# Kernel optimization log

Measured on AMD Instinct MI355X. Metric: run time of the kernel, lower is better.

Reference implementation:

```python
import jax, jax.numpy as jnp
import numpy as np

T, K, E, D, F = 2048, 6, 32, 2048, 1408   # tokens, top_k, routed experts, dim, moe_inter_dim
S = 2                                      # fused shared experts
C = T * K // E                             # exact per-expert capacity (balanced routing)


def _silu_and_mul(gu):
    # merged gate_up activation: silu(gate_half) * up_half
    g, u = jnp.split(gu, 2, axis=-1)
    return jax.nn.silu(g) * u


def setup_inputs() -> dict:
    key = jax.random.key(0)
    ks = jax.random.split(key, 7)
    x = jax.random.normal(ks[0], (T, D), dtype=jnp.float32)
    # balanced routing: every expert receives exactly C = T*K/E token-expert pairs
    indices = jax.random.permutation(ks[1], jnp.arange(T * K, dtype=jnp.int32) % E).reshape(T, K)
    weights = jax.random.uniform(ks[2], (T, K), dtype=jnp.float32)
    scale = 0.02
    w_gate_up = jax.random.normal(ks[3], (E, D, 2 * F), dtype=jnp.float32) * scale
    w_down = jax.random.normal(ks[4], (E, F, D), dtype=jnp.float32) * scale
    w_gate_up_shared = jax.random.normal(ks[5], (S, D, 2 * F), dtype=jnp.float32) * scale
    w_down_shared = jax.random.normal(ks[6], (S, F, D), dtype=jnp.float32) * scale
    return {"x": x, "weights": weights, "w_gate_up": w_gate_up, "w_down": w_down,
            "w_gate_up_shared": w_gate_up_shared, "w_down_shared": w_down_shared,
            "indices": indices}


def reference(x, weights, w_gate_up, w_down, w_gate_up_shared, w_down_shared, indices):
    # ---- dispatch: sort token-expert pairs by expert id (balanced -> exactly C per expert)
    flat_e = indices.reshape(-1)                       # [T*K]
    order = jnp.argsort(flat_e, stable=True)           # [T*K] pair ids grouped by expert
    tok = order // K                                   # source token of each sorted pair
    w_sorted = weights.reshape(-1)[order]              # routing weight of each sorted pair
    xg = x[tok].reshape(E, C, D)                       # gathered per-expert inputs
    # ---- routed experts: grouped gate_up GEMM -> silu_and_mul -> down GEMM
    act = _silu_and_mul(jnp.einsum('ecd,edf->ecf', xg, w_gate_up))   # [E, C, F]
    down = jnp.einsum('ecf,efd->ecd', act, w_down)                   # [E, C, D]
    # ---- combine: weighted scatter-add back to token order (y[idx] += out * weights[idx, top])
    y = jnp.zeros_like(x).at[tok].add(down.reshape(E * C, D) * w_sorted[:, None])
    # ---- fused shared experts: run on all tokens, added unweighted
    act_s = _silu_and_mul(jnp.einsum('td,sdf->stf', x, w_gate_up_shared))  # [S, T, F]
    y = y + jnp.einsum('stf,sfd->td', act_s, w_down_shared)
    return y
```

## Files before the change

kernel.cpp:

```cpp
#include <hip/hip_runtime.h>
#include <hip/hip_bf16.h>

#define TT 2048
#define KK 6
#define EE 32
#define DD 2048
#define FF 1408
#define SS 2
#define CC 384

typedef __bf16 bf16_t;
typedef __attribute__((ext_vector_type(8))) __bf16 bf16x8;
typedef __attribute__((ext_vector_type(4))) float f32x4;
typedef unsigned int u32;

#define AS1 __attribute__((address_space(1)))
#define AS3 __attribute__((address_space(3)))

__device__ __forceinline__ u32 f2bf(float f) {
    u32 u = __builtin_bit_cast(u32, f);
    return (u + 0x7fffu + ((u >> 16) & 1u)) >> 16;
}
__device__ __forceinline__ u32 pack2(float a, float b) {
    return f2bf(a) | (f2bf(b) << 16);
}
__device__ __forceinline__ float silu_mul(float g, float u) {
    return (g / (1.0f + __expf(-g))) * u;
}

__global__ void k_dispatch(const int* __restrict__ idx, int* __restrict__ counts,
                           int* __restrict__ tok, int* __restrict__ sop) {
    int p = blockIdx.x * 256 + threadIdx.x;
    if (p >= TT * KK) return;
    int e = idx[p];
    int pos = atomicAdd(&counts[e], 1);
    int slot = e * CC + pos;
    tok[slot] = p / KK;
    sop[p] = slot;
}

__global__ void k_gather(const float* __restrict__ x, const int* __restrict__ tok,
                         bf16_t* __restrict__ xall) {
    int row = blockIdx.x;
    int srow = (row < EE * CC) ? tok[row] : (row - EE * CC);
    const float* src = x + (size_t)srow * DD;
    bf16_t* dst = xall + (size_t)row * DD;
    int c0 = threadIdx.x * 8;
    float4 a = *(const float4*)(src + c0);
    float4 b = *(const float4*)(src + c0 + 4);
    uint4 o;
    o.x = pack2(a.x, a.y); o.y = pack2(a.z, a.w);
    o.z = pack2(b.x, b.y); o.w = pack2(b.z, b.w);
    *(uint4*)(dst + c0) = o;
}

#define BSTR 40

__device__ __forceinline__ void stage_a6(const bf16_t* __restrict__ A, int Kdim, int k0,
                                         bf16_t* dst, int arow, int ac, int wid) {
    #pragma unroll
    for (int i = 0; i < 6; ++i) {
        const int row = i * 64 + arow;
        const int cs = ac ^ ((row >> 1) & 3);
        const bf16_t* g = A + (size_t)row * Kdim + (k0 + cs * 8);
        AS3 u32* l = (AS3 u32*)(void*)(dst + (size_t)(i * 64 + wid * 16) * 32);
        __builtin_amdgcn_global_load_lds((const AS1 u32*)(const void*)g, l, 16, 0, 0);
    }
}

template<bool FUSED>
__global__ __launch_bounds__(256) void k_gemm_r(
    const bf16_t* __restrict__ Aall, const float* __restrict__ Br,
    bf16_t* __restrict__ Out, int Kdim, int Bstr, int Ostr, int NB)
{
    const int lin = blockIdx.x;
    const int xcd = lin & 7, jj = lin >> 3;
    const int e = xcd + 8 * (jj / NB);
    const int nblk = jj % NB;

    const bf16_t* A = Aall + (size_t)e * CC * Kdim;
    const float* Bbase = Br + (size_t)e * Kdim * Bstr;

    const int tid = threadIdx.x;
    const int lane = tid & 63, wid = tid >> 6;
    const int m_base = wid * 96;
    const int l15 = lane & 15, lq = lane >> 4;
    const int arow = tid >> 2, ac = tid & 3;
    const int kb = (tid >> 6) * 8;
    const int bn = tid & 63;

    const float* bsrc;
    bf16_t* Cout;
    if (FUSED) {
        const float* Bg = Bbase + nblk * 32;
        bsrc = (((tid >> 5) & 1) ? (Bg + FF) : Bg) + (tid & 31);
        Cout = Out + (size_t)e * CC * Ostr + nblk * 32;
    } else {
        bsrc = Bbase + nblk * 64 + bn;
        Cout = Out + (size_t)e * CC * Ostr + nblk * 64;
    }

    __shared__ __align__(16) bf16_t As[2][CC * 32];
    __shared__ __align__(16) bf16_t Bs[2][64 * BSTR];

    f32x4 acc[6][4] = {};
    const int ksteps = Kdim >> 5;

    auto loadB = [&](int k0, float* v) {
        const float* sp = bsrc + (size_t)(k0 + kb) * Bstr;
        #pragma unroll
        for (int t = 0; t < 8; ++t) v[t] = sp[(size_t)t * Bstr];
    };
    auto writeB = [&](int b, const float* v) {
        uint4 w;
        w.x = pack2(v[0], v[1]); w.y = pack2(v[2], v[3]);
        w.z = pack2(v[4], v[5]); w.w = pack2(v[6], v[7]);
        *(uint4*)(&Bs[b][0] + (size_t)bn * BSTR + kb) = w;
    };

    {
        stage_a6(A, Kdim, 0, &As[0][0], arow, ac, wid);
        float v[8]; loadB(0, v); writeB(0, v);
    }
    __syncthreads();

    int cur = 0;
    for (int kt = 0; kt < ksteps; ++kt) {
        const bool pf = (kt + 1 < ksteps);
        float vn[8];
        if (pf) {
            const int k1 = (kt + 1) << 5;
            stage_a6(A, Kdim, k1, &As[cur ^ 1][0], arow, ac, wid);
            loadB(k1, vn);
        }
        bf16x8 bfr[4];
        #pragma unroll
        for (int j = 0; j < 4; ++j)
            bfr[j] = *(const bf16x8*)(&Bs[cur][0] + (size_t)(j * 16 + l15) * BSTR + lq * 8);
        #pragma unroll
        for (int m = 0; m < 6; ++m) {
            const int row = m_base + m * 16 + l15;
            bf16x8 af = *(const bf16x8*)(&As[cur][0] + (size_t)row * 32 + (size_t)((lq ^ ((row >> 1) & 3)) * 8));
            #pragma unroll
            for (int j = 0; j < 4; ++j)
                acc[m][j] = __builtin_amdgcn_mfma_f32_16x16x32_bf16(af, bfr[j], acc[m][j], 0, 0, 0);
        }
        if (pf) writeB(cur ^ 1, vn);
        __syncthreads();
        cur ^= 1;
    }

    if (FUSED) {
        #pragma unroll
        for (int m = 0; m < 6; ++m)
            #pragma unroll
            for (int j = 0; j < 2; ++j) {
                const int n = j * 16 + l15;
                #pragma unroll
                for (int r = 0; r < 4; ++r) {
                    const int mm = m_base + m * 16 + lq * 4 + r;
                    Cout[(size_t)mm * Ostr + n] = (bf16_t)silu_mul(acc[m][j][r], acc[m][j + 2][r]);
                }
            }
    } else {
        #pragma unroll
        for (int m = 0; m < 6; ++m)
            #pragma unroll
            for (int j = 0; j < 4; ++j) {
                const int n = j * 16 + l15;
                #pragma unroll
                for (int r = 0; r < 4; ++r) {
                    const int mm = m_base + m * 16 + lq * 4 + r;
                    Cout[(size_t)mm * Ostr + n] = (bf16_t)acc[m][j][r];
                }
            }
    }
}

template<bool FUSED>
__global__ __launch_bounds__(256) void k_gemm_s(
    const bf16_t* __restrict__ Ash, const float* __restrict__ Bsh,
    bf16_t* __restrict__ Out, int Kdim, int Bstr, int Ostr, int ash_stride)
{
    const int s = blockIdx.z;
    const int n0 = blockIdx.x * (FUSED ? 64 : 128);
    const bf16_t* A = Ash + ((size_t)s * ash_stride + (size_t)blockIdx.y * 128) * Kdim;
    bf16_t* Cout = Out + ((size_t)s * TT + (size_t)blockIdx.y * 128) * Ostr + n0;
    const float* Bbase = Bsh + (size_t)s * Kdim * Bstr + n0;

    const int tid = threadIdx.x;
    const int lane = tid & 63, wid = tid >> 6;
    const int m_off = (wid >> 1) * 64, wn = wid & 1;
    const int l15 = lane & 15, lq = lane >> 4;
    const int arow = tid >> 2, ac = tid & 3;
    const int bn = tid & 127, kb = (tid >> 7) * 16;

    const float* bsrc;
    if (FUSED) bsrc = (((tid >> 6) & 1) ? (Bbase + FF) : Bbase) + (tid & 63);
    else       bsrc = Bbase + bn;

    __shared__ __align__(16) bf16_t As[2][128 * 32];
    __shared__ __align__(16) bf16_t Bs[2][128 * BSTR];

    f32x4 acc[4][4] = {};
    const int ksteps = Kdim >> 5;

    auto stageA = [&](int b, int k0) {
        const int cs = ac ^ ((arow >> 1) & 3);
        const bf16_t* g0 = A + (size_t)arow * Kdim + (k0 + cs * 8);
        const bf16_t* g1 = A + (size_t)(arow + 64) * Kdim + (k0 + cs * 8);
        AS3 u32* l0 = (AS3 u32*)(void*)(&As[b][0] + (size_t)(wid * 16) * 32);
        AS3 u32* l1 = (AS3 u32*)(void*)(&As[b][0] + (size_t)(64 + wid * 16) * 32);
        __builtin_amdgcn_global_load_lds((const AS1 u32*)(const void*)g0, l0, 16, 0, 0);
        __builtin_amdgcn_global_load_lds((const AS1 u32*)(const void*)g1, l1, 16, 0, 0);
    };
    auto loadB = [&](int k0, float* v) {
        const float* sp = bsrc + (size_t)(k0 + kb) * Bstr;
        #pragma unroll
        for (int t = 0; t < 16; ++t) v[t] = sp[(size_t)t * Bstr];
    };
    auto writeB = [&](int b, const float* v) {
        u32 p[8];
        #pragma unroll
        for (int t = 0; t < 8; ++t) p[t] = pack2(v[2 * t], v[2 * t + 1]);
        uint4 w0, w1;
        w0.x = p[0]; w0.y = p[1]; w0.z = p[2]; w0.w = p[3];
        w1.x = p[4]; w1.y = p[5]; w1.z = p[6]; w1.w = p[7];
        *(uint4*)(&Bs[b][0] + (size_t)bn * BSTR + kb) = w0;
        *(uint4*)(&Bs[b][0] + (size_t)bn * BSTR + kb + 8) = w1;
    };

    {
        stageA(0, 0);
        float v[16]; loadB(0, v); writeB(0, v);
    }
    __syncthreads();

    int cur = 0;
    for (int kt = 0; kt < ksteps; ++kt) {
        const bool pf = (kt + 1 < ksteps);
        float vn[16];
        if (pf) {
            const int k1 = (kt + 1) << 5;
            stageA(cur ^ 1, k1);
            loadB(k1, vn);
        }
        bf16x8 af[4], bfr[4];
        #pragma unroll
        for (int i = 0; i < 4; ++i) {
            const int row = m_off + i * 16 + l15;
            af[i] = *(const bf16x8*)(&As[cur][0] + (size_t)row * 32 + (size_t)((lq ^ ((row >> 1) & 3)) * 8));
        }
        #pragma unroll
        for (int j = 0; j < 4; ++j) {
            const int n_ds = FUSED ? (wn * 32 + (j & 1) * 16 + (j >> 1) * 64)
                                   : (wn * 64 + j * 16);
            bfr[j] = *(const bf16x8*)(&Bs[cur][0] + (size_t)(n_ds + l15) * BSTR + lq * 8);
        }
        #pragma unroll
        for (int i = 0; i < 4; ++i)
            #pragma unroll
            for (int j = 0; j < 4; ++j)
                acc[i][j] = __builtin_amdgcn_mfma_f32_16x16x32_bf16(af[i], bfr[j], acc[i][j], 0, 0, 0);
        if (pf) writeB(cur ^ 1, vn);
        __syncthreads();
        cur ^= 1;
    }

    if (FUSED) {
        #pragma unroll
        for (int i = 0; i < 4; ++i)
            #pragma unroll
            for (int j = 0; j < 2; ++j) {
                const int n = wn * 32 + j * 16 + l15;
                #pragma unroll
                for (int r = 0; r < 4; ++r) {
                    const int m = m_off + i * 16 + lq * 4 + r;
                    Cout[(size_t)m * Ostr + n] = (bf16_t)silu_mul(acc[i][j][r], acc[i][j + 2][r]);
                }
            }
    } else {
        #pragma unroll
        for (int i = 0; i < 4; ++i)
            #pragma unroll
            for (int j = 0; j < 4; ++j) {
                const int n = wn * 64 + j * 16 + l15;
                #pragma unroll
                for (int r = 0; r < 4; ++r) {
                    const int m = m_off + i * 16 + lq * 4 + r;
                    Cout[(size_t)m * Ostr + n] = (bf16_t)acc[i][j][r];
                }
            }
    }
}

__global__ void k_combine(const bf16_t* __restrict__ down, const int* __restrict__ sop,
                          const float* __restrict__ wts, float* __restrict__ y) {
    int t = blockIdx.x;
    int d0 = threadIdx.x * 8;
    float a[8] = {0, 0, 0, 0, 0, 0, 0, 0};
    #pragma unroll
    for (int k = 0; k < KK; ++k) {
        int slot = sop[t * KK + k];
        float w = wts[t * KK + k];
        bf16x8 v = *(const bf16x8*)(down + (size_t)slot * DD + d0);
        #pragma unroll
        for (int j = 0; j < 8; ++j) a[j] += w * (float)v[j];
    }
    #pragma unroll
    for (int s = 0; s < SS; ++s) {
        bf16x8 v = *(const bf16x8*)(down + ((size_t)EE * CC + (size_t)s * TT + t) * DD + d0);
        #pragma unroll
        for (int j = 0; j < 8; ++j) a[j] += (float)v[j];
    }
    float4 o0, o1;
    o0.x = a[0]; o0.y = a[1]; o0.z = a[2]; o0.w = a[3];
    o1.x = a[4]; o1.y = a[5]; o1.z = a[6]; o1.w = a[7];
    *(float4*)(y + (size_t)t * DD + d0) = o0;
    *(float4*)(y + (size_t)t * DD + d0 + 4) = o1;
}

extern "C" void kernel_launch(void* const* d_in, const int* in_sizes, int n_in,
                              void* d_out, int out_size, void* d_ws, size_t ws_size,
                              hipStream_t stream) {
    (void)in_sizes; (void)n_in; (void)out_size; (void)ws_size;
    const float* x      = (const float*)d_in[0];
    const float* wts    = (const float*)d_in[1];
    const float* w_gu   = (const float*)d_in[2];
    const float* w_dn   = (const float*)d_in[3];
    const float* w_gu_s = (const float*)d_in[4];
    const float* w_dn_s = (const float*)d_in[5];
    const int*   indices= (const int*)d_in[6];
    float* y = (float*)d_out;

    char* ws = (char*)d_ws;
    size_t off = 0;
    auto alloc = [&](size_t bytes) {
        void* p = ws + off;
        off = (off + bytes + 255) & ~(size_t)255;
        return p;
    };
    int*    counts = (int*)alloc((size_t)EE * 4);
    int*    tok    = (int*)alloc((size_t)EE * CC * 4);
    int*    sop    = (int*)alloc((size_t)TT * KK * 4);
    bf16_t* xall   = (bf16_t*)alloc((size_t)(EE * CC + TT) * DD * 2);
    bf16_t* actb   = (bf16_t*)alloc((size_t)(EE * CC + SS * TT) * FF * 2);
    bf16_t* dnout  = (bf16_t*)alloc((size_t)(EE * CC + SS * TT) * DD * 2);

    hipMemsetAsync(counts, 0, EE * 4, stream);
    k_dispatch<<<(TT * KK + 255) / 256, 256, 0, stream>>>(indices, counts, tok, sop);
    k_gather<<<EE * CC + TT, 256, 0, stream>>>(x, tok, xall);

    k_gemm_r<true><<<44 * EE, 256, 0, stream>>>(xall, w_gu, actb, DD, 2 * FF, FF, 44);
    k_gemm_s<true><<<dim3(FF / 64, TT / 128, SS), 256, 0, stream>>>(
        xall + (size_t)EE * CC * DD, w_gu_s, actb + (size_t)EE * CC * FF, DD, 2 * FF, FF, 0);

    k_gemm_r<false><<<32 * EE, 256, 0, stream>>>(actb, w_dn, dnout, FF, DD, DD, 32);
    k_gemm_s<false><<<dim3(DD / 128, TT / 128, SS), 256, 0, stream>>>(
        actb + (size_t)EE * CC * FF, w_dn_s, dnout + (size_t)EE * CC * DD, FF, DD, DD, TT);

    k_combine<<<TT, 256, 0, stream>>>(dnout, sop, wts, y);
}
```

Before: 1.590 ms.

## Widen routed GEMM tiles to 512 threads with triple-buffered A and manual waitcnt pipelining

The routed-expert GEMM now uses 512-thread blocks covering twice the N width per block, so each staged A tile of 384 rows is reused across more output columns. Both routed and shared GEMMs switch to a triple-buffered A ring with double-buffered B, using explicit s_waitcnt vmcnt/lgkmcnt counts and raw barriers so loads for step k+2 overlap compute on step k. The shared GEMM grid is also remapped so blocks that share a weight column land on the same XCD. The gain comes at the cost of more LDS per block and hand-tuned wait counts that break silently if the load counts change.

```diff
diff --git a/kernel.cpp b/kernel.cpp
--- a/kernel.cpp
+++ b/kernel.cpp
@@ -56,20 +56,8 @@
 
 #define BSTR 40
 
-__device__ __forceinline__ void stage_a6(const bf16_t* __restrict__ A, int Kdim, int k0,
-                                         bf16_t* dst, int arow, int ac, int wid) {
-    #pragma unroll
-    for (int i = 0; i < 6; ++i) {
-        const int row = i * 64 + arow;
-        const int cs = ac ^ ((row >> 1) & 3);
-        const bf16_t* g = A + (size_t)row * Kdim + (k0 + cs * 8);
-        AS3 u32* l = (AS3 u32*)(void*)(dst + (size_t)(i * 64 + wid * 16) * 32);
-        __builtin_amdgcn_global_load_lds((const AS1 u32*)(const void*)g, l, 16, 0, 0);
-    }
-}
-
 template<bool FUSED>
-__global__ __launch_bounds__(256) void k_gemm_r(
+__global__ __launch_bounds__(512) void k_gemm_r(
     const bf16_t* __restrict__ Aall, const float* __restrict__ Br,
     bf16_t* __restrict__ Out, int Kdim, int Bstr, int Ostr, int NB)
 {
@@ -83,79 +71,117 @@
 
     const int tid = threadIdx.x;
     const int lane = tid & 63, wid = tid >> 6;
-    const int m_base = wid * 96;
+    const int m_base = (wid >> 1) * 96, wn = wid & 1;
     const int l15 = lane & 15, lq = lane >> 4;
     const int arow = tid >> 2, ac = tid & 3;
-    const int kb = (tid >> 6) * 8;
-    const int bn = tid & 63;
+    const int bn = tid & 127, kb = (tid >> 7) * 8;
 
     const float* bsrc;
     bf16_t* Cout;
     if (FUSED) {
-        const float* Bg = Bbase + nblk * 32;
-        bsrc = (((tid >> 5) & 1) ? (Bg + FF) : Bg) + (tid & 31);
-        Cout = Out + (size_t)e * CC * Ostr + nblk * 32;
+        bsrc = Bbase + ((bn & 64) ? FF : 0) + nblk * 64 + (bn & 63);
+        Cout = Out + (size_t)e * CC * Ostr + nblk * 64;
     } else {
-        bsrc = Bbase + nblk * 64 + bn;
-        Cout = Out + (size_t)e * CC * Ostr + nblk * 64;
-    }
-
-    __shared__ __align__(16) bf16_t As[2][CC * 32];
-    __shared__ __align__(16) bf16_t Bs[2][64 * BSTR];
+        bsrc = Bbase + nblk * 128 + bn;
+        Cout = Out + (size_t)e * CC * Ostr + nblk * 128;
+    }
+
+    __shared__ __align__(16) bf16_t As[3][384 * 32];
+    __shared__ __align__(16) bf16_t Bs[2][128 * BSTR];
 
     f32x4 acc[6][4] = {};
     const int ksteps = Kdim >> 5;
 
-    auto loadB = [&](int k0, float* v) {
-        const float* sp = bsrc + (size_t)(k0 + kb) * Bstr;
+    auto stageA = [&](int kt, bf16_t* dst) {
+        const int k0 = kt << 5;
+        #pragma unroll
+        for (int i = 0; i < 3; ++i) {
+            const int row = i * 128 + arow;
+            const int cs = ac ^ ((row >> 1) & 3);
+            const bf16_t* g = A + (size_t)row * Kdim + (k0 + cs * 8);
+            AS3 u32* l = (AS3 u32*)(void*)(dst + (size_t)(i * 128 + wid * 16) * 32);
+            __builtin_amdgcn_global_load_lds((const AS1 u32*)(const void*)g, l, 16, 0, 0);
+        }
+    };
+    auto loadB = [&](int kt, float* v) {
+        const float* sp = bsrc + (size_t)((kt << 5) + kb) * Bstr;
         #pragma unroll
         for (int t = 0; t < 8; ++t) v[t] = sp[(size_t)t * Bstr];
     };
-    auto writeB = [&](int b, const float* v) {
+    auto writeB = [&](bf16_t* bbuf, const float* v) {
         uint4 w;
         w.x = pack2(v[0], v[1]); w.y = pack2(v[2], v[3]);
         w.z = pack2(v[4], v[5]); w.w = pack2(v[6], v[7]);
-        *(uint4*)(&Bs[b][0] + (size_t)bn * BSTR + kb) = w;
-    };
-
-    {
-        stage_a6(A, Kdim, 0, &As[0][0], arow, ac, wid);
-        float v[8]; loadB(0, v); writeB(0, v);
-    }
-    __syncthreads();
-
-    int cur = 0;
-    for (int kt = 0; kt < ksteps; ++kt) {
-        const bool pf = (kt + 1 < ksteps);
-        float vn[8];
-        if (pf) {
-            const int k1 = (kt + 1) << 5;
-            stage_a6(A, Kdim, k1, &As[cur ^ 1][0], arow, ac, wid);
-            loadB(k1, vn);
-        }
+        *(uint4*)(bbuf + (size_t)bn * BSTR + kb) = w;
+    };
+    auto compute = [&](const bf16_t* abuf, const bf16_t* bbuf) {
         bf16x8 bfr[4];
         #pragma unroll
-        for (int j = 0; j < 4; ++j)
-            bfr[j] = *(const bf16x8*)(&Bs[cur][0] + (size_t)(j * 16 + l15) * BSTR + lq * 8);
+        for (int j = 0; j < 4; ++j) {
+            const int n_ds = FUSED ? (wn * 32 + (j & 1) * 16 + (j >> 1) * 64)
+                                   : (wn * 64 + j * 16);
+            bfr[j] = *(const bf16x8*)(bbuf + (size_t)(n_ds + l15) * BSTR + lq * 8);
+        }
         #pragma unroll
         for (int m = 0; m < 6; ++m) {
             const int row = m_base + m * 16 + l15;
-            bf16x8 af = *(const bf16x8*)(&As[cur][0] + (size_t)row * 32 + (size_t)((lq ^ ((row >> 1) & 3)) * 8));
+            bf16x8 af = *(const bf16x8*)(abuf + (size_t)row * 32 + (size_t)((lq ^ ((row >> 1) & 3)) * 8));
             #pragma unroll
             for (int j = 0; j < 4; ++j)
                 acc[m][j] = __builtin_amdgcn_mfma_f32_16x16x32_bf16(af, bfr[j], acc[m][j], 0, 0, 0);
         }
-        if (pf) writeB(cur ^ 1, vn);
-        __syncthreads();
-        cur ^= 1;
-    }
+    };
+
+    float vBa[8], vBb[8];
+    bf16_t *aR = &As[0][0], *aS = &As[1][0], *aT = &As[2][0];
+
+    loadB(0, vBa);
+    stageA(0, aR);
+    asm volatile("s_waitcnt vmcnt(3)" ::: "memory");
+    writeB(&Bs[0][0], vBa);
+    loadB(1, vBb);
+    stageA(1, aS);
+    asm volatile("s_waitcnt lgkmcnt(0)" ::: "memory");
+    __builtin_amdgcn_s_barrier();
+
+    for (int t = 0; t < ksteps - 2; t += 2) {
+        loadB(t + 2, vBa);
+        asm volatile("s_waitcnt vmcnt(19)" ::: "memory");
+        asm volatile("s_waitcnt lgkmcnt(0)" ::: "memory");
+        __builtin_amdgcn_s_barrier();
+        stageA(t + 2, aT);
+        compute(aR, &Bs[0][0]);
+        asm volatile("s_waitcnt vmcnt(14)" ::: "memory");
+        writeB(&Bs[1][0], vBb);
+        { bf16_t* tmp = aR; aR = aS; aS = aT; aT = tmp; }
+        loadB(t + 3, vBb);
+        asm volatile("s_waitcnt vmcnt(19)" ::: "memory");
+        asm volatile("s_waitcnt lgkmcnt(0)" ::: "memory");
+        __builtin_amdgcn_s_barrier();
+        stageA(t + 3, aT);
+        compute(aR, &Bs[1][0]);
+        asm volatile("s_waitcnt vmcnt(14)" ::: "memory");
+        writeB(&Bs[0][0], vBa);
+        { bf16_t* tmp = aR; aR = aS; aS = aT; aT = tmp; }
+    }
+
+    asm volatile("s_waitcnt vmcnt(11)" ::: "memory");
+    asm volatile("s_waitcnt lgkmcnt(0)" ::: "memory");
+    __builtin_amdgcn_s_barrier();
+    compute(aR, &Bs[0][0]);
+    asm volatile("s_waitcnt vmcnt(3)" ::: "memory");
+    writeB(&Bs[1][0], vBb);
+    asm volatile("s_waitcnt vmcnt(0)" ::: "memory");
+    asm volatile("s_waitcnt lgkmcnt(0)" ::: "memory");
+    __builtin_amdgcn_s_barrier();
+    compute(aS, &Bs[1][0]);
 
     if (FUSED) {
         #pragma unroll
         for (int m = 0; m < 6; ++m)
             #pragma unroll
             for (int j = 0; j < 2; ++j) {
-                const int n = j * 16 + l15;
+                const int n = wn * 32 + j * 16 + l15;
                 #pragma unroll
                 for (int r = 0; r < 4; ++r) {
                     const int mm = m_base + m * 16 + lq * 4 + r;
@@ -167,7 +193,7 @@
         for (int m = 0; m < 6; ++m)
             #pragma unroll
             for (int j = 0; j < 4; ++j) {
-                const int n = j * 16 + l15;
+                const int n = wn * 64 + j * 16 + l15;
                 #pragma unroll
                 for (int r = 0; r < 4; ++r) {
                     const int mm = m_base + m * 16 + lq * 4 + r;
@@ -180,13 +206,18 @@
 template<bool FUSED>
 __global__ __launch_bounds__(256) void k_gemm_s(
     const bf16_t* __restrict__ Ash, const float* __restrict__ Bsh,
-    bf16_t* __restrict__ Out, int Kdim, int Bstr, int Ostr, int ash_stride)
+    bf16_t* __restrict__ Out, int Kdim, int Bstr, int Ostr, int ash_stride,
+    int nkeys, int KQ, int NBs)
 {
-    const int s = blockIdx.z;
-    const int n0 = blockIdx.x * (FUSED ? 64 : 128);
-    const bf16_t* A = Ash + ((size_t)s * ash_stride + (size_t)blockIdx.y * 128) * Kdim;
-    bf16_t* Cout = Out + ((size_t)s * TT + (size_t)blockIdx.y * 128) * Ostr + n0;
-    const float* Bbase = Bsh + (size_t)s * Kdim * Bstr + n0;
+    const int b = blockIdx.x;
+    const int xcd = b & 7, jj = b >> 3;
+    const int m = jj / KQ, kq = jj % KQ;
+    const int key = kq * 8 + xcd;
+    if (key >= nkeys) return;
+    const int s = key / NBs, nb = key % NBs;
+
+    const bf16_t* A = Ash + ((size_t)s * ash_stride + (size_t)m * 128) * Kdim;
+    const float* Bp = Bsh + (size_t)s * Kdim * Bstr;
 
     const int tid = threadIdx.x;
     const int lane = tid & 63, wid = tid >> 6;
@@ -196,76 +227,110 @@
     const int bn = tid & 127, kb = (tid >> 7) * 16;
 
     const float* bsrc;
-    if (FUSED) bsrc = (((tid >> 6) & 1) ? (Bbase + FF) : Bbase) + (tid & 63);
-    else       bsrc = Bbase + bn;
-
-    __shared__ __align__(16) bf16_t As[2][128 * 32];
+    bf16_t* Cout;
+    if (FUSED) {
+        bsrc = Bp + (((tid >> 6) & 1) ? FF : 0) + nb * 64 + (tid & 63);
+        Cout = Out + ((size_t)s * TT + (size_t)m * 128) * Ostr + nb * 64;
+    } else {
+        bsrc = Bp + nb * 128 + bn;
+        Cout = Out + ((size_t)s * TT + (size_t)m * 128) * Ostr + nb * 128;
+    }
+
+    __shared__ __align__(16) bf16_t As[3][128 * 32];
     __shared__ __align__(16) bf16_t Bs[2][128 * BSTR];
 
     f32x4 acc[4][4] = {};
     const int ksteps = Kdim >> 5;
 
-    auto stageA = [&](int b, int k0) {
-        const int cs = ac ^ ((arow >> 1) & 3);
-        const bf16_t* g0 = A + (size_t)arow * Kdim + (k0 + cs * 8);
-        const bf16_t* g1 = A + (size_t)(arow + 64) * Kdim + (k0 + cs * 8);
-        AS3 u32* l0 = (AS3 u32*)(void*)(&As[b][0] + (size_t)(wid * 16) * 32);
-        AS3 u32* l1 = (AS3 u32*)(void*)(&As[b][0] + (size_t)(64 + wid * 16) * 32);
-        __builtin_amdgcn_global_load_lds((const AS1 u32*)(const void*)g0, l0, 16, 0, 0);
-        __builtin_amdgcn_global_load_lds((const AS1 u32*)(const void*)g1, l1, 16, 0, 0);
-    };
-    auto loadB = [&](int k0, float* v) {
-        const float* sp = bsrc + (size_t)(k0 + kb) * Bstr;
+    auto stageA = [&](int kt, bf16_t* dst) {
+        const int k0 = kt << 5;
+        #pragma unroll
+        for (int i = 0; i < 2; ++i) {
+            const int row = i * 64 + arow;
+            const int cs = ac ^ ((row >> 1) & 3);
+            const bf16_t* g = A + (size_t)row * Kdim + (k0 + cs * 8);
+            AS3 u32* l = (AS3 u32*)(void*)(dst + (size_t)(i * 64 + wid * 16) * 32);
+            __builtin_amdgcn_global_load_lds((const AS1 u32*)(const void*)g, l, 16, 0, 0);
+        }
+    };
+    auto loadB = [&](int kt, float* v) {
+        const float* sp = bsrc + (size_t)((kt << 5) + kb) * Bstr;
         #pragma unroll
         for (int t = 0; t < 16; ++t) v[t] = sp[(size_t)t * Bstr];
     };
-    auto writeB = [&](int b, const float* v) {
+    auto writeB = [&](bf16_t* bbuf, const float* v) {
         u32 p[8];
         #pragma unroll
         for (int t = 0; t < 8; ++t) p[t] = pack2(v[2 * t], v[2 * t + 1]);
         uint4 w0, w1;
         w0.x = p[0]; w0.y = p[1]; w0.z = p[2]; w0.w = p[3];
         w1.x = p[4]; w1.y = p[5]; w1.z = p[6]; w1.w = p[7];
-        *(uint4*)(&Bs[b][0] + (size_t)bn * BSTR + kb) = w0;
-        *(uint4*)(&Bs[b][0] + (size_t)bn * BSTR + kb + 8) = w1;
-    };
-
-    {
-        stageA(0, 0);
-        float v[16]; loadB(0, v); writeB(0, v);
-    }
-    __syncthreads();
-
-    int cur = 0;
-    for (int kt = 0; kt < ksteps; ++kt) {
-        const bool pf = (kt + 1 < ksteps);
-        float vn[16];
-        if (pf) {
-            const int k1 = (kt + 1) << 5;
-            stageA(cur ^ 1, k1);
-            loadB(k1, vn);
-        }
+        *(uint4*)(bbuf + (size_t)bn * BSTR + kb) = w0;
+        *(uint4*)(bbuf + (size_t)bn * BSTR + kb + 8) = w1;
+    };
+    auto compute = [&](const bf16_t* abuf, const bf16_t* bbuf) {
         bf16x8 af[4], bfr[4];
         #pragma unroll
         for (int i = 0; i < 4; ++i) {
             const int row = m_off + i * 16 + l15;
-            af[i] = *(const bf16x8*)(&As[cur][0] + (size_t)row * 32 + (size_t)((lq ^ ((row >> 1) & 3)) * 8));
+            af[i] = *(const bf16x8*)(abuf + (size_t)row * 32 + (size_t)((lq ^ ((row >> 1) & 3)) * 8));
         }
         #pragma unroll
         for (int j = 0; j < 4; ++j) {
             const int n_ds = FUSED ? (wn * 32 + (j & 1) * 16 + (j >> 1) * 64)
                                    : (wn * 64 + j * 16);
-            bfr[j] = *(const bf16x8*)(&Bs[cur][0] + (size_t)(n_ds + l15) * BSTR + lq * 8);
+            bfr[j] = *(const bf16x8*)(bbuf + (size_t)(n_ds + l15) * BSTR + lq * 8);
         }
         #pragma unroll
         for (int i = 0; i < 4; ++i)
             #pragma unroll
             for (int j = 0; j < 4; ++j)
                 acc[i][j] = __builtin_amdgcn_mfma_f32_16x16x32_bf16(af[i], bfr[j], acc[i][j], 0, 0, 0);
-        if (pf) writeB(cur ^ 1, vn);
-        __syncthreads();
-        cur ^= 1;
-    }
+    };
+
+    float vBa[16], vBb[16];
+    bf16_t *aR = &As[0][0], *aS = &As[1][0], *aT = &As[2][0];
+
+    loadB(0, vBa);
+    stageA(0, aR);
+    asm volatile("s_waitcnt vmcnt(2)" ::: "memory");
+    writeB(&Bs[0][0], vBa);
+    loadB(1, vBb);
+    stageA(1, aS);
+    asm volatile("s_waitcnt lgkmcnt(0)" ::: "memory");
+    __builtin_amdgcn_s_barrier();
+
+    for (int t = 0; t < ksteps - 2; t += 2) {
+        loadB(t + 2, vBa);
+        asm volatile("s_waitcnt vmcnt(34)" ::: "memory");
+        asm volatile("s_waitcnt lgkmcnt(0)" ::: "memory");
+        __builtin_amdgcn_s_barrier();
+        stageA(t + 2, aT);
+        compute(aR, &Bs[0][0]);
+        asm volatile("s_waitcnt vmcnt(20)" ::: "memory");
+        writeB(&Bs[1][0], vBb);
+        { bf16_t* tmp = aR; aR = aS; aS = aT; aT = tmp; }
+        loadB(t + 3, vBb);
+        asm volatile("s_waitcnt vmcnt(34)" ::: "memory");
+        asm volatile("s_waitcnt lgkmcnt(0)" ::: "memory");
+        __builtin_amdgcn_s_barrier();
+        stageA(t + 3, aT);
+        compute(aR, &Bs[1][0]);
+        asm volatile("s_waitcnt vmcnt(20)" ::: "memory");
+        writeB(&Bs[0][0], vBa);
+        { bf16_t* tmp = aR; aR = aS; aS = aT; aT = tmp; }
+    }
+
+    asm volatile("s_waitcnt vmcnt(18)" ::: "memory");
+    asm volatile("s_waitcnt lgkmcnt(0)" ::: "memory");
+    __builtin_amdgcn_s_barrier();
+    compute(aR, &Bs[0][0]);
+    asm volatile("s_waitcnt vmcnt(2)" ::: "memory");
+    writeB(&Bs[1][0], vBb);
+    asm volatile("s_waitcnt vmcnt(0)" ::: "memory");
+    asm volatile("s_waitcnt lgkmcnt(0)" ::: "memory");
+    __builtin_amdgcn_s_barrier();
+    compute(aS, &Bs[1][0]);
 
     if (FUSED) {
         #pragma unroll
@@ -275,8 +340,8 @@
                 const int n = wn * 32 + j * 16 + l15;
                 #pragma unroll
                 for (int r = 0; r < 4; ++r) {
-                    const int m = m_off + i * 16 + lq * 4 + r;
-                    Cout[(size_t)m * Ostr + n] = (bf16_t)silu_mul(acc[i][j][r], acc[i][j + 2][r]);
+                    const int mm = m_off + i * 16 + lq * 4 + r;
+                    Cout[(size_t)mm * Ostr + n] = (bf16_t)silu_mul(acc[i][j][r], acc[i][j + 2][r]);
                 }
             }
     } else {
@@ -287,8 +352,8 @@
                 const int n = wn * 64 + j * 16 + l15;
                 #pragma unroll
                 for (int r = 0; r < 4; ++r) {
-                    const int m = m_off + i * 16 + lq * 4 + r;
-                    Cout[(size_t)m * Ostr + n] = (bf16_t)acc[i][j][r];
+                    const int mm = m_off + i * 16 + lq * 4 + r;
+                    Cout[(size_t)mm * Ostr + n] = (bf16_t)acc[i][j][r];
                 }
             }
     }
@@ -351,13 +416,15 @@
     k_dispatch<<<(TT * KK + 255) / 256, 256, 0, stream>>>(indices, counts, tok, sop);
     k_gather<<<EE * CC + TT, 256, 0, stream>>>(x, tok, xall);
 
-    k_gemm_r<true><<<44 * EE, 256, 0, stream>>>(xall, w_gu, actb, DD, 2 * FF, FF, 44);
-    k_gemm_s<true><<<dim3(FF / 64, TT / 128, SS), 256, 0, stream>>>(
-        xall + (size_t)EE * CC * DD, w_gu_s, actb + (size_t)EE * CC * FF, DD, 2 * FF, FF, 0);
-
-    k_gemm_r<false><<<32 * EE, 256, 0, stream>>>(actb, w_dn, dnout, FF, DD, DD, 32);
-    k_gemm_s<false><<<dim3(DD / 128, TT / 128, SS), 256, 0, stream>>>(
-        actb + (size_t)EE * CC * FF, w_dn_s, dnout + (size_t)EE * CC * DD, FF, DD, DD, TT);
+    k_gemm_r<true><<<EE * 22, 512, 0, stream>>>(xall, w_gu, actb, DD, 2 * FF, FF, 22);
+    k_gemm_s<true><<<8 * 6 * 16, 256, 0, stream>>>(
+        xall + (size_t)EE * CC * DD, w_gu_s, actb + (size_t)EE * CC * FF,
+        DD, 2 * FF, FF, 0, 44, 6, 22);
+
+    k_gemm_r<false><<<EE * 16, 512, 0, stream>>>(actb, w_dn, dnout, FF, DD, DD, 16);
+    k_gemm_s<false><<<8 * 4 * 16, 256, 0, stream>>>(
+        actb + (size_t)EE * CC * FF, w_dn_s, dnout + (size_t)EE * CC * DD,
+        FF, DD, DD, TT, 32, 4, 16);
 
     k_combine<<<TT, 256, 0, stream>>>(dnout, sop, wts, y);
 }
```

Result: faster. 1.485 ms (-6.6%).
